# Optimization experiments

Hardware: AMD Instinct MI355X
Metric: run time of the kernel (lower is better)

## Reference

```python
import jax, jax.numpy as jnp
import numpy as np

N_NODES = 100000
N_EDGES = 1600000
D_IN = 128
D_OUT = 128


def setup_inputs() -> dict:
    key = jax.random.key(0)
    k1, k2, k3, k4, k5 = jax.random.split(key, 5)
    x = jax.random.normal(k1, (N_NODES, D_IN), dtype=jnp.float32)
    x_0 = jax.random.normal(k2, (N_NODES, D_IN), dtype=jnp.float32)
    edge_index = jax.random.randint(k3, (2, N_EDGES), 0, N_NODES, dtype=jnp.int64)
    # GCNConv linear weight (glorot-ish scale) and bias
    W = jax.random.normal(k4, (D_IN, D_OUT), dtype=jnp.float32) / np.sqrt(D_IN)
    b = jax.random.normal(k5, (D_OUT,), dtype=jnp.float32) * 0.01
    return {"x": x, "x_0": x_0, "W": W, "b": b, "edge_index": edge_index}


def reference(x, x_0, W, b, edge_index):
    # SemiGCNConv.forward: relu(GCNConv(x, edge_index)); x_0 is unused.
    N = x.shape[0]
    # GCNConv default: add self-loops, symmetric normalization
    loop = jnp.arange(N, dtype=edge_index.dtype)
    src = jnp.concatenate([edge_index[0], loop])  # [E+N]
    dst = jnp.concatenate([edge_index[1], loop])  # [E+N]
    # degree of target nodes (edge_weight = 1)
    deg = jax.ops.segment_sum(jnp.ones_like(dst, dtype=x.dtype), dst, num_segments=N)
    deg_inv_sqrt = jnp.where(deg > 0, jax.lax.rsqrt(deg), 0.0)
    norm = deg_inv_sqrt[src] * deg_inv_sqrt[dst]  # [E+N]
    # linear transform first (PyG order), then normalized scatter-add aggregation
    h = x @ W  # [N, D_OUT]
    msg = h[src] * norm[:, None]  # gather + scale, [E+N, D_OUT]
    out = jax.ops.segment_sum(msg, dst, num_segments=N) + b
    return jax.nn.relu(out)
```

## Files before the change

kernel.cpp:

```cpp
#include <hip/hip_runtime.h>

#define N_NODES 100000
#define N_EDGES 1600000
#define D 128
#define G 256
#define NB 391
#define NB_PAD 392
#define CAP 6144
#define EPT 16

typedef __attribute__((ext_vector_type(8))) short bf16x8;
typedef __attribute__((ext_vector_type(4))) float f32x4;

__device__ inline float bf2f(unsigned short u) {
    return __uint_as_float(((unsigned int)u) << 16);
}
__device__ inline unsigned short f2bf(float f) {
    unsigned int u = __float_as_uint(f);
    unsigned int r = u + 0x7FFF + ((u >> 16) & 1);
    return (unsigned short)(r >> 16);
}

__device__ inline int wave_incl_scan(int v, int lane) {
    #pragma unroll
    for (int off = 1; off < 64; off <<= 1) {
        int y = __shfl_up(v, off);
        if (lane >= off) v += y;
    }
    return v;
}

__global__ __launch_bounds__(256) void bin_edges(const int* __restrict__ ei,
                                                 int* __restrict__ gcursor,
                                                 unsigned int* __restrict__ bins) {
    __shared__ int hist[NB_PAD];
    __shared__ int base[NB_PAD];
    const int tid = threadIdx.x;
    for (int i = tid; i < NB; i += 256) hist[i] = 0;
    __syncthreads();

    const long long e0 = (long long)blockIdx.x * (256 * EPT) + (long long)tid * EPT;
    const bool active = (e0 < N_EDGES);
    unsigned int packed[EPT]; int bkt[EPT]; int rnk[EPT];
    if (active) {
        const int4* s4 = (const int4*)(ei + e0);
        const int4* d4 = (const int4*)(ei + N_EDGES + e0);
        #pragma unroll
        for (int q = 0; q < EPT / 4; ++q) {
            int4 s = s4[q], d = d4[q];
            int j = q * 4;
            bkt[j+0] = d.x >> 8; packed[j+0] = (unsigned)s.x | ((unsigned)(d.x & 255) << 17);
            bkt[j+1] = d.y >> 8; packed[j+1] = (unsigned)s.y | ((unsigned)(d.y & 255) << 17);
            bkt[j+2] = d.z >> 8; packed[j+2] = (unsigned)s.z | ((unsigned)(d.z & 255) << 17);
            bkt[j+3] = d.w >> 8; packed[j+3] = (unsigned)s.w | ((unsigned)(d.w & 255) << 17);
        }
        #pragma unroll
        for (int j = 0; j < EPT; ++j) rnk[j] = atomicAdd(&hist[bkt[j]], 1);
    }
    __syncthreads();
    for (int i = tid; i < NB; i += 256) {
        int c = hist[i];
        base[i] = c ? atomicAdd(&gcursor[i], c) : 0;
    }
    __syncthreads();
    if (active) {
        #pragma unroll
        for (int j = 0; j < EPT; ++j) {
            int pos = base[bkt[j]] + rnk[j];
            if (pos < CAP) bins[(size_t)bkt[j] * CAP + pos] = packed[j];
        }
    }
}

__global__ __launch_bounds__(512) void scan_buckets(const int* __restrict__ gcursor,
                                                    int* __restrict__ bucket_base) {
    __shared__ int wtot[8];
    int t = threadIdx.x, lane = t & 63, w = t >> 6;
    int v = (t < NB) ? gcursor[t] : 0;
    int incl = wave_incl_scan(v, lane);
    if (lane == 63) wtot[w] = incl;
    __syncthreads();
    int add = 0;
    for (int i = 0; i < w; ++i) add += wtot[i];
    if (t < NB) bucket_base[t] = incl - v + add;
}

__global__ __launch_bounds__(256) void bucket_csr(const unsigned int* __restrict__ bins,
                                                  const int* __restrict__ gcursor,
                                                  const int* __restrict__ bucket_base,
                                                  int* __restrict__ deg,
                                                  float* __restrict__ dinv,
                                                  int* __restrict__ row_start,
                                                  int* __restrict__ csr) {
    __shared__ int degL[G];
    __shared__ int rsL[G];
    __shared__ int curL[G];
    __shared__ int wq[4];
    __shared__ int csrL[CAP];
    const int b = blockIdx.x, t = threadIdx.x;
    int cb = gcursor[b];
    if (cb > CAP) cb = CAP;
    const int ebase = bucket_base[b];
    degL[t] = 0;
    __syncthreads();
    const unsigned int* mybins = bins + (size_t)b * CAP;
    for (int i = t; i < cb; i += 256)
        atomicAdd(&degL[(mybins[i] >> 17) & 255], 1);
    __syncthreads();
    int v = degL[t];
    int incl = wave_incl_scan(v, t & 63);
    if ((t & 63) == 63) wq[t >> 6] = incl;
    __syncthreads();
    int add = 0;
    for (int i = 0; i < (t >> 6); ++i) add += wq[i];
    int ex = incl - v + add;
    rsL[t] = ex;
    curL[t] = 0;
    int node = b * G + t;
    if (node < N_NODES) {
        deg[node] = v;
        dinv[node] = rsqrtf((float)v + 1.0f);
        row_start[node] = ebase + ex;
    }
    __syncthreads();
    for (int i = t; i < cb; i += 256) {
        unsigned int u = mybins[i];
        int dl = (u >> 17) & 255;
        int pos = rsL[dl] + atomicAdd(&curL[dl], 1);
        csrL[pos] = (int)(u & 0x1FFFF);
    }
    __syncthreads();
    for (int i = t; i < cb; i += 256) csr[ebase + i] = csrL[i];
}

__global__ __launch_bounds__(512) void gemm_h_mfma(
        const float* __restrict__ x, const float* __restrict__ W,
        const float* __restrict__ dinv, unsigned short* __restrict__ h) {
    __shared__ unsigned short wt[D * D];
    const int tid  = threadIdx.x;
    const int lane = tid & 63;
    const int wv   = tid >> 6;
    const int rb   = blockIdx.x * 128 + wv * 16;

    int arow = rb + (lane & 15);
    if (arow >= N_NODES) arow = N_NODES - 1;
    const float4* xrow = (const float4*)(x + (size_t)arow * D);
    float4 af[8];
    #pragma unroll
    for (int kt = 0; kt < 4; ++kt) {
        int fi = kt * 8 + (lane >> 4) * 2;
        af[kt * 2]     = xrow[fi];
        af[kt * 2 + 1] = xrow[fi + 1];
    }

    const float4* W4 = (const float4*)W;
    float4 wreg[8];
    #pragma unroll
    for (int i = 0; i < 8; ++i) wreg[i] = W4[tid + 512 * i];
    #pragma unroll
    for (int i = 0; i < 8; ++i) {
        int idx = tid + 512 * i;
        int k  = idx >> 5;
        int c0 = (idx & 31) * 4;
        float v[4] = {wreg[i].x, wreg[i].y, wreg[i].z, wreg[i].w};
        #pragma unroll
        for (int j = 0; j < 4; ++j) {
            int c = c0 + j;
            int byte = (c * 256 + k * 2) ^ ((c & 7) << 4);
            *(unsigned short*)((char*)wt + byte) = f2bf(v[j]);
        }
    }
    __syncthreads();

    bf16x8 a[4];
    #pragma unroll
    for (int kt = 0; kt < 4; ++kt) {
        float4 u = af[kt * 2], v = af[kt * 2 + 1];
        a[kt][0] = (short)f2bf(u.x); a[kt][1] = (short)f2bf(u.y);
        a[kt][2] = (short)f2bf(u.z); a[kt][3] = (short)f2bf(u.w);
        a[kt][4] = (short)f2bf(v.x); a[kt][5] = (short)f2bf(v.y);
        a[kt][6] = (short)f2bf(v.z); a[kt][7] = (short)f2bf(v.w);
    }

    f32x4 acc[8];
    #pragma unroll
    for (int ct = 0; ct < 8; ++ct) acc[ct] = (f32x4){0.f, 0.f, 0.f, 0.f};

    const int cbase = lane & 15;
    const int kgrp  = (lane >> 4) * 8;
    #pragma unroll
    for (int ct = 0; ct < 8; ++ct) {
        int c = ct * 16 + cbase;
        #pragma unroll
        for (int kt = 0; kt < 4; ++kt) {
            int byte = (c * 256 + (kt * 32 + kgrp) * 2) ^ ((c & 7) << 4);
            bf16x8 bfr = *(const bf16x8*)((const char*)wt + byte);
            acc[ct] = __builtin_amdgcn_mfma_f32_16x16x32_bf16(a[kt], bfr, acc[ct], 0, 0, 0);
        }
    }

    float dq[4]; int orow[4];
    #pragma unroll
    for (int q = 0; q < 4; ++q) {
        orow[q] = rb + (lane >> 4) * 4 + q;
        dq[q] = dinv[orow[q] < N_NODES ? orow[q] : 0];
    }
    #pragma unroll
    for (int ct = 0; ct < 8; ++ct) {
        int col = ct * 16 + (lane & 15);
        #pragma unroll
        for (int q = 0; q < 4; ++q) {
            if (orow[q] < N_NODES)
                h[(size_t)orow[q] * D + col] = f2bf(acc[ct][q] * dq[q]);
        }
    }
}

__global__ __launch_bounds__(256) void gather_out(const int* __restrict__ csr,
                                                  const int* __restrict__ row_start,
                                                  const int* __restrict__ deg,
                                                  const float* __restrict__ dinv,
                                                  const ushort4* __restrict__ h4,
                                                  const float4* __restrict__ b4,
                                                  float4* __restrict__ out4) {
    int tid = threadIdx.x;
    int c = tid & 31;
    int n = blockIdx.x * 8 + (tid >> 5);
    if (n >= N_NODES) return;
    ushort4 hv = h4[(size_t)n * 32 + c];
    float4 acc = {bf2f(hv.x), bf2f(hv.y), bf2f(hv.z), bf2f(hv.w)};
    int rs = row_start[n], dg = deg[n];
    for (int base = 0; base < dg; base += 32) {
        int m = min(32, dg - base);
        int src = 0;
        if (c < m) src = csr[rs + base + c];
        for (int j = 0; j < m; ++j) {
            int s = __shfl(src, j, 32);
            ushort4 v = h4[(size_t)s * 32 + c];
            acc.x += bf2f(v.x); acc.y += bf2f(v.y);
            acc.z += bf2f(v.z); acc.w += bf2f(v.w);
        }
    }
    float di = dinv[n];
    float4 bb = b4[c];
    float4 o;
    o.x = fmaxf(fmaf(di, acc.x, bb.x), 0.f);
    o.y = fmaxf(fmaf(di, acc.y, bb.y), 0.f);
    o.z = fmaxf(fmaf(di, acc.z, bb.z), 0.f);
    o.w = fmaxf(fmaf(di, acc.w, bb.w), 0.f);
    out4[(size_t)n * 32 + c] = o;
}

extern "C" void kernel_launch(void* const* d_in, const int* in_sizes, int n_in,
                              void* d_out, int out_size, void* d_ws, size_t ws_size,
                              hipStream_t stream) {
    const float* x  = (const float*)d_in[0];
    const float* W  = (const float*)d_in[2];
    const float* b  = (const float*)d_in[3];
    const int*   ei = (const int*)d_in[4];
    float* out = (float*)d_out;

    unsigned short* h = (unsigned short*)d_ws;
    int*   deg         = (int*)(h + (size_t)N_NODES * D);
    float* dinv        = (float*)(deg + N_NODES);
    int*   row_start   = (int*)(dinv + N_NODES);
    int*   gcursor     = row_start + N_NODES;
    int*   bucket_base = gcursor + NB_PAD;
    int*   csr         = bucket_base + NB_PAD;
    unsigned int* bins = (unsigned int*)(csr + N_EDGES);

    hipMemsetAsync(gcursor, 0, NB_PAD * sizeof(int), stream);

    bin_edges<<<(N_EDGES + 256 * EPT - 1) / (256 * EPT), 256, 0, stream>>>(ei, gcursor, bins);
    scan_buckets<<<1, 512, 0, stream>>>(gcursor, bucket_base);
    bucket_csr<<<NB, 256, 0, stream>>>(bins, gcursor, bucket_base, deg, dinv, row_start, csr);
    gemm_h_mfma<<<(N_NODES + 127) / 128, 512, 0, stream>>>(x, W, dinv, h);
    gather_out<<<(N_NODES + 7) / 8, 256, 0, stream>>>(csr, row_start, deg, dinv,
                                                      (const ushort4*)h,
                                                      (const float4*)b, (float4*)out);
}
```

Measured before the change: 257.7 us.

## Fuse bucket CSR build into gather and count degrees with global atomics

Shrinks destination buckets to 64 nodes, computes per-node degree with global atomics inside the binning kernel, and drops the scan and global CSR kernels. Each gather block now builds its bucket's local CSR in shared memory and aggregates straight from it, with the inner gather loop unrolled by four. This removes two launches and the global CSR/row_start round trip. In exchange it adds 1.6M scattered global atomics, and gather parallelism is fixed at 8 nodes per 256-thread block with serialized local CSR construction. Bucket capacity is tighter (1536 for an average of about 1024), so heavily loaded buckets are more likely to be truncated.

```diff
diff --git a/kernel.cpp b/kernel.cpp
--- a/kernel.cpp
+++ b/kernel.cpp
@@ -3,10 +3,10 @@
 #define N_NODES 100000
 #define N_EDGES 1600000
 #define D 128
-#define G 256
-#define NB 391
-#define NB_PAD 392
-#define CAP 6144
+#define G 64
+#define NB 1563
+#define NB_PAD 1568
+#define CAP 1536
 #define EPT 16
 
 typedef __attribute__((ext_vector_type(8))) short bf16x8;
@@ -30,11 +30,12 @@
     return v;
 }
 
-__global__ __launch_bounds__(256) void bin_edges(const int* __restrict__ ei,
+__global__ __launch_bounds__(256) void bin_count(const int* __restrict__ ei,
+                                                 int* __restrict__ deg,
                                                  int* __restrict__ gcursor,
                                                  unsigned int* __restrict__ bins) {
-    __shared__ int hist[NB_PAD];
-    __shared__ int base[NB_PAD];
+    __shared__ int hist[NB];
+    __shared__ int base[NB];
     const int tid = threadIdx.x;
     for (int i = tid; i < NB; i += 256) hist[i] = 0;
     __syncthreads();
@@ -49,10 +50,14 @@
         for (int q = 0; q < EPT / 4; ++q) {
             int4 s = s4[q], d = d4[q];
             int j = q * 4;
-            bkt[j+0] = d.x >> 8; packed[j+0] = (unsigned)s.x | ((unsigned)(d.x & 255) << 17);
-            bkt[j+1] = d.y >> 8; packed[j+1] = (unsigned)s.y | ((unsigned)(d.y & 255) << 17);
-            bkt[j+2] = d.z >> 8; packed[j+2] = (unsigned)s.z | ((unsigned)(d.z & 255) << 17);
-            bkt[j+3] = d.w >> 8; packed[j+3] = (unsigned)s.w | ((unsigned)(d.w & 255) << 17);
+            bkt[j+0] = d.x >> 6; packed[j+0] = (unsigned)s.x | ((unsigned)(d.x & 63) << 17);
+            bkt[j+1] = d.y >> 6; packed[j+1] = (unsigned)s.y | ((unsigned)(d.y & 63) << 17);
+            bkt[j+2] = d.z >> 6; packed[j+2] = (unsigned)s.z | ((unsigned)(d.z & 63) << 17);
+            bkt[j+3] = d.w >> 6; packed[j+3] = (unsigned)s.w | ((unsigned)(d.w & 63) << 17);
+            atomicAdd(&deg[d.x], 1);
+            atomicAdd(&deg[d.y], 1);
+            atomicAdd(&deg[d.z], 1);
+            atomicAdd(&deg[d.w], 1);
         }
         #pragma unroll
         for (int j = 0; j < EPT; ++j) rnk[j] = atomicAdd(&hist[bkt[j]], 1);
@@ -72,70 +77,9 @@
     }
 }
 
-__global__ __launch_bounds__(512) void scan_buckets(const int* __restrict__ gcursor,
-                                                    int* __restrict__ bucket_base) {
-    __shared__ int wtot[8];
-    int t = threadIdx.x, lane = t & 63, w = t >> 6;
-    int v = (t < NB) ? gcursor[t] : 0;
-    int incl = wave_incl_scan(v, lane);
-    if (lane == 63) wtot[w] = incl;
-    __syncthreads();
-    int add = 0;
-    for (int i = 0; i < w; ++i) add += wtot[i];
-    if (t < NB) bucket_base[t] = incl - v + add;
-}
-
-__global__ __launch_bounds__(256) void bucket_csr(const unsigned int* __restrict__ bins,
-                                                  const int* __restrict__ gcursor,
-                                                  const int* __restrict__ bucket_base,
-                                                  int* __restrict__ deg,
-                                                  float* __restrict__ dinv,
-                                                  int* __restrict__ row_start,
-                                                  int* __restrict__ csr) {
-    __shared__ int degL[G];
-    __shared__ int rsL[G];
-    __shared__ int curL[G];
-    __shared__ int wq[4];
-    __shared__ int csrL[CAP];
-    const int b = blockIdx.x, t = threadIdx.x;
-    int cb = gcursor[b];
-    if (cb > CAP) cb = CAP;
-    const int ebase = bucket_base[b];
-    degL[t] = 0;
-    __syncthreads();
-    const unsigned int* mybins = bins + (size_t)b * CAP;
-    for (int i = t; i < cb; i += 256)
-        atomicAdd(&degL[(mybins[i] >> 17) & 255], 1);
-    __syncthreads();
-    int v = degL[t];
-    int incl = wave_incl_scan(v, t & 63);
-    if ((t & 63) == 63) wq[t >> 6] = incl;
-    __syncthreads();
-    int add = 0;
-    for (int i = 0; i < (t >> 6); ++i) add += wq[i];
-    int ex = incl - v + add;
-    rsL[t] = ex;
-    curL[t] = 0;
-    int node = b * G + t;
-    if (node < N_NODES) {
-        deg[node] = v;
-        dinv[node] = rsqrtf((float)v + 1.0f);
-        row_start[node] = ebase + ex;
-    }
-    __syncthreads();
-    for (int i = t; i < cb; i += 256) {
-        unsigned int u = mybins[i];
-        int dl = (u >> 17) & 255;
-        int pos = rsL[dl] + atomicAdd(&curL[dl], 1);
-        csrL[pos] = (int)(u & 0x1FFFF);
-    }
-    __syncthreads();
-    for (int i = t; i < cb; i += 256) csr[ebase + i] = csrL[i];
-}
-
 __global__ __launch_bounds__(512) void gemm_h_mfma(
         const float* __restrict__ x, const float* __restrict__ W,
-        const float* __restrict__ dinv, unsigned short* __restrict__ h) {
+        const int* __restrict__ deg, unsigned short* __restrict__ h) {
     __shared__ unsigned short wt[D * D];
     const int tid  = threadIdx.x;
     const int lane = tid & 63;
@@ -203,7 +147,8 @@
     #pragma unroll
     for (int q = 0; q < 4; ++q) {
         orow[q] = rb + (lane >> 4) * 4 + q;
-        dq[q] = dinv[orow[q] < N_NODES ? orow[q] : 0];
+        int rr = orow[q] < N_NODES ? orow[q] : 0;
+        dq[q] = rsqrtf((float)deg[rr] + 1.0f);
     }
     #pragma unroll
     for (int ct = 0; ct < 8; ++ct) {
@@ -216,39 +161,73 @@
     }
 }
 
-__global__ __launch_bounds__(256) void gather_out(const int* __restrict__ csr,
-                                                  const int* __restrict__ row_start,
-                                                  const int* __restrict__ deg,
-                                                  const float* __restrict__ dinv,
-                                                  const ushort4* __restrict__ h4,
-                                                  const float4* __restrict__ b4,
-                                                  float4* __restrict__ out4) {
-    int tid = threadIdx.x;
-    int c = tid & 31;
-    int n = blockIdx.x * 8 + (tid >> 5);
-    if (n >= N_NODES) return;
-    ushort4 hv = h4[(size_t)n * 32 + c];
-    float4 acc = {bf2f(hv.x), bf2f(hv.y), bf2f(hv.z), bf2f(hv.w)};
-    int rs = row_start[n], dg = deg[n];
-    for (int base = 0; base < dg; base += 32) {
-        int m = min(32, dg - base);
-        int src = 0;
-        if (c < m) src = csr[rs + base + c];
-        for (int j = 0; j < m; ++j) {
-            int s = __shfl(src, j, 32);
+__global__ __launch_bounds__(256) void bucket_gather(const unsigned int* __restrict__ bins,
+                                                     const int* __restrict__ gcursor,
+                                                     const ushort4* __restrict__ h4,
+                                                     const float4* __restrict__ b4,
+                                                     float4* __restrict__ out4) {
+    __shared__ int degL[G];
+    __shared__ int rsL[G];
+    __shared__ int curL[G];
+    __shared__ int csrL[CAP];
+    const int b = blockIdx.x, t = threadIdx.x;
+    int cb = gcursor[b];
+    if (cb > CAP) cb = CAP;
+    if (t < G) { degL[t] = 0; curL[t] = 0; }
+    __syncthreads();
+    const unsigned int* mybins = bins + (size_t)b * CAP;
+    for (int i = t; i < cb; i += 256)
+        atomicAdd(&degL[(mybins[i] >> 17) & 63], 1);
+    __syncthreads();
+    if (t < G) {
+        int v = degL[t];
+        int incl = wave_incl_scan(v, t);
+        rsL[t] = incl - v;
+    }
+    __syncthreads();
+    for (int i = t; i < cb; i += 256) {
+        unsigned int u = mybins[i];
+        int dl = (u >> 17) & 63;
+        int pos = rsL[dl] + atomicAdd(&curL[dl], 1);
+        csrL[pos] = (int)(u & 0x1FFFF);
+    }
+    __syncthreads();
+
+    const int c = t & 31, g = t >> 5;
+    for (int nl = g; nl < G; nl += 8) {
+        int node = b * G + nl;
+        if (node >= N_NODES) break;
+        int rs = rsL[nl], dg = degL[nl];
+        ushort4 hv = h4[(size_t)node * 32 + c];
+        float4 acc = {bf2f(hv.x), bf2f(hv.y), bf2f(hv.z), bf2f(hv.w)};
+        int j = 0;
+        for (; j + 4 <= dg; j += 4) {
+            int s0 = csrL[rs + j], s1 = csrL[rs + j + 1];
+            int s2 = csrL[rs + j + 2], s3 = csrL[rs + j + 3];
+            ushort4 v0 = h4[(size_t)s0 * 32 + c];
+            ushort4 v1 = h4[(size_t)s1 * 32 + c];
+            ushort4 v2 = h4[(size_t)s2 * 32 + c];
+            ushort4 v3 = h4[(size_t)s3 * 32 + c];
+            acc.x += bf2f(v0.x) + bf2f(v1.x) + bf2f(v2.x) + bf2f(v3.x);
+            acc.y += bf2f(v0.y) + bf2f(v1.y) + bf2f(v2.y) + bf2f(v3.y);
+            acc.z += bf2f(v0.z) + bf2f(v1.z) + bf2f(v2.z) + bf2f(v3.z);
+            acc.w += bf2f(v0.w) + bf2f(v1.w) + bf2f(v2.w) + bf2f(v3.w);
+        }
+        for (; j < dg; ++j) {
+            int s = csrL[rs + j];
             ushort4 v = h4[(size_t)s * 32 + c];
             acc.x += bf2f(v.x); acc.y += bf2f(v.y);
             acc.z += bf2f(v.z); acc.w += bf2f(v.w);
         }
-    }
-    float di = dinv[n];
-    float4 bb = b4[c];
-    float4 o;
-    o.x = fmaxf(fmaf(di, acc.x, bb.x), 0.f);
-    o.y = fmaxf(fmaf(di, acc.y, bb.y), 0.f);
-    o.z = fmaxf(fmaf(di, acc.z, bb.z), 0.f);
-    o.w = fmaxf(fmaf(di, acc.w, bb.w), 0.f);
-    out4[(size_t)n * 32 + c] = o;
+        float dn = rsqrtf((float)dg + 1.0f);
+        float4 bb = b4[c];
+        float4 o;
+        o.x = fmaxf(fmaf(dn, acc.x, bb.x), 0.f);
+        o.y = fmaxf(fmaf(dn, acc.y, bb.y), 0.f);
+        o.z = fmaxf(fmaf(dn, acc.z, bb.z), 0.f);
+        o.w = fmaxf(fmaf(dn, acc.w, bb.w), 0.f);
+        out4[(size_t)node * 32 + c] = o;
+    }
 }
 
 extern "C" void kernel_launch(void* const* d_in, const int* in_sizes, int n_in,
@@ -260,22 +239,15 @@
     const int*   ei = (const int*)d_in[4];
     float* out = (float*)d_out;
 
-    unsigned short* h = (unsigned short*)d_ws;
+    unsigned short* h  = (unsigned short*)d_ws;
     int*   deg         = (int*)(h + (size_t)N_NODES * D);
-    float* dinv        = (float*)(deg + N_NODES);
-    int*   row_start   = (int*)(dinv + N_NODES);
-    int*   gcursor     = row_start + N_NODES;
-    int*   bucket_base = gcursor + NB_PAD;
-    int*   csr         = bucket_base + NB_PAD;
-    unsigned int* bins = (unsigned int*)(csr + N_EDGES);
-
-    hipMemsetAsync(gcursor, 0, NB_PAD * sizeof(int), stream);
-
-    bin_edges<<<(N_EDGES + 256 * EPT - 1) / (256 * EPT), 256, 0, stream>>>(ei, gcursor, bins);
-    scan_buckets<<<1, 512, 0, stream>>>(gcursor, bucket_base);
-    bucket_csr<<<NB, 256, 0, stream>>>(bins, gcursor, bucket_base, deg, dinv, row_start, csr);
-    gemm_h_mfma<<<(N_NODES + 127) / 128, 512, 0, stream>>>(x, W, dinv, h);
-    gather_out<<<(N_NODES + 7) / 8, 256, 0, stream>>>(csr, row_start, deg, dinv,
-                                                      (const ushort4*)h,
-                                                      (const float4*)b, (float4*)out);
-}
+    int*   gcursor     = deg + N_NODES;
+    unsigned int* bins = (unsigned int*)(gcursor + NB_PAD);
+
+    hipMemsetAsync(deg, 0, (N_NODES + NB_PAD) * sizeof(int), stream);
+
+    bin_count<<<(N_EDGES + 256 * EPT - 1) / (256 * EPT), 256, 0, stream>>>(ei, deg, gcursor, bins);
+    gemm_h_mfma<<<(N_NODES + 127) / 128, 512, 0, stream>>>(x, W, deg, h);
+    bucket_gather<<<NB, 256, 0, stream>>>(bins, gcursor, (const ushort4*)h,
+                                          (const float4*)b, (float4*)out);
+}
```

New measurement: 294.9 us. 14.5% more time.
